# Kernel optimization log

Measured on AMD Instinct MI355X. Metric: run time of the kernel, lower is better.

The kernel has to match this reference:

```python
import jax, jax.numpy as jnp
import numpy as np

B, R, K, S = 512, 264, 32, 9
SUB_ENDS = np.array([28, 58, 92, 121, 150, 180, 210, 240, 264], dtype=np.int32)


def setup_inputs() -> dict:
    key = jax.random.key(0)
    embeddings = jax.random.normal(key, (B, R, K), dtype=jnp.float32)
    return {"embeddings": embeddings, "subnetwork_ends": jnp.asarray(SUB_ENDS)}


def reference(embeddings, subnetwork_ends):
    # subnetwork_ends are static structural constants (cumulative block ends).
    ends = np.asarray(jax.device_get(subnetwork_ends))
    starts = np.concatenate([np.zeros(1, dtype=ends.dtype), ends[:-1]])
    sizes = ends - starts                      # [S]
    n_sub = ends.shape[0]
    seg = np.repeat(np.arange(n_sub), sizes)   # [R] segment id per ROI

    # adjacency: batched gram matrix, [B, R, R]
    adjacency = jnp.einsum('brk,bpk->brp', embeddings, embeddings)

    # intra-network adjacency: zero out cross-block entries
    intra_mask = jnp.asarray(seg[:, None] == seg[None, :])  # [R, R] bool
    intra = adjacency * intra_mask                          # [B, R, R]

    # inter-network matrix: block means via one fused segment reduce
    # (replaces the O(S^2) per-block slice+mean loop in the original)
    one_hot = jnp.asarray(np.eye(n_sub, dtype=np.float32)[seg])          # [R, S]
    counts = jnp.asarray((sizes[:, None] * sizes[None, :]).astype(np.float32))  # [S, S]
    inter = jnp.einsum('brp,rs,pt->bst', adjacency, one_hot, one_hot) / counts  # [B, S, S]

    return intra[..., None], inter[..., None], adjacency[..., None]
```

## Files before the change

### kernel.cpp

```cpp
#include <hip/hip_runtime.h>


constexpr int B_ = 512, R_ = 264, K_ = 32, S_ = 9;
constexpr int RP_ = 292;
constexpr long long NI_ = (long long)B_ * R_ * R_;
constexpr long long NS_ = (long long)B_ * S_ * S_;

typedef float vf4 __attribute__((ext_vector_type(4)));

__global__ __launch_bounds__(576, 8) void adj_intra(
    const float* __restrict__ emb, float* __restrict__ out) {
  __shared__ float Et[K_ * RP_];
  __shared__ unsigned char seg_lut[288];

  const int b = blockIdx.x;
  const int stripe = blockIdx.y;
  const int tid = threadIdx.x;
  const float* __restrict__ eb = emb + (size_t)b * R_ * K_;

  for (int idx = tid; idx < (R_ * K_) / 4; idx += 576) {
    const int r = idx >> 3;
    const int kq = (idx & 7) * 4;
    const vf4 v = *reinterpret_cast<const vf4*>(eb + r * K_ + kq);
    Et[(kq + 0) * RP_ + r] = v.x;
    Et[(kq + 1) * RP_ + r] = v.y;
    Et[(kq + 2) * RP_ + r] = v.z;
    Et[(kq + 3) * RP_ + r] = v.w;
  }
  for (int z = tid; z < K_ * 24; z += 576) {
    const int k = z / 24, r = 264 + z % 24;
    Et[k * RP_ + r] = 0.0f;
  }
  if (tid < 288) {
    const int x = tid;
    seg_lut[x] = (x >= 28) + (x >= 58) + (x >= 92) + (x >= 121) +
                 (x >= 150) + (x >= 180) + (x >= 210) + (x >= 240);
  }
  __syncthreads();

  const int wave = tid >> 6, lane = tid & 63;
  const int lx = lane & 7, ly = lane >> 3;
  const int i0 = stripe * 32 + ly * 4;
  const int j0 = wave * 32 + lx * 4;

  vf4 acc0 = {0, 0, 0, 0}, acc1 = {0, 0, 0, 0};
  vf4 acc2 = {0, 0, 0, 0}, acc3 = {0, 0, 0, 0};
#pragma unroll 4
  for (int k = 0; k < K_; ++k) {
    const vf4 av = *reinterpret_cast<const vf4*>(Et + k * RP_ + i0);
    const vf4 bv = *reinterpret_cast<const vf4*>(Et + k * RP_ + j0);
    acc0 += av.x * bv;
    acc1 += av.y * bv;
    acc2 += av.z * bv;
    acc3 += av.w * bv;
  }

  if (j0 < R_) {
    float* __restrict__ intra_out = out;
    float* __restrict__ adj_out = out + NI_ + NS_;
    const int sj0 = seg_lut[j0], sj1 = seg_lut[j0 + 1];
    const int sj2 = seg_lut[j0 + 2], sj3 = seg_lut[j0 + 3];
    const size_t base = (size_t)b * R_ * R_ + (size_t)j0;
    const vf4 accs[4] = {acc0, acc1, acc2, acc3};
#pragma unroll
    for (int ii = 0; ii < 4; ++ii) {
      const int i = i0 + ii;
      if (i < R_) {
        const vf4 v = accs[ii];
        const int si = seg_lut[i];
        vf4 m;
        m.x = (si == sj0) ? v.x : 0.0f;
        m.y = (si == sj1) ? v.y : 0.0f;
        m.z = (si == sj2) ? v.z : 0.0f;
        m.w = (si == sj3) ? v.w : 0.0f;
        const size_t idx = base + (size_t)i * R_;
        __builtin_nontemporal_store(v, reinterpret_cast<vf4*>(adj_out + idx));
        __builtin_nontemporal_store(m, reinterpret_cast<vf4*>(intra_out + idx));
      }
    }
  }
}

__global__ __launch_bounds__(256) void inter_k(
    const float* __restrict__ emb, float* __restrict__ out) {
  constexpr int ENDS[S_] = {28, 58, 92, 121, 150, 180, 210, 240, 264};
  constexpr int STARTS[S_] = {0, 28, 58, 92, 121, 150, 180, 210, 240};
  constexpr float SZ[S_] = {28.f, 30.f, 34.f, 29.f, 29.f, 30.f, 30.f, 30.f, 24.f};

  __shared__ float ps[S_ * 8 * 32];
  __shared__ float ss[32 * 12];

  const int b = blockIdx.x, tid = threadIdx.x;
  const int k = tid & 31, q = tid >> 5;
  const float* __restrict__ eb = emb + (size_t)b * R_ * K_;

#pragma unroll
  for (int s = 0; s < S_; ++s) {
    const int lo = STARTS[s], len = ENDS[s] - STARTS[s];
    const int c0 = lo + (len * q) / 8, c1 = lo + (len * (q + 1)) / 8;
    float a = 0.0f;
    for (int r = c0; r < c1; ++r) a += eb[r * K_ + k];
    ps[(s * 8 + q) * 32 + k] = a;
  }
  __syncthreads();
  for (int c = tid; c < S_ * 32; c += 256) {
    const int s = c >> 5, kk = c & 31;
    float a = 0.0f;
#pragma unroll
    for (int qq = 0; qq < 8; ++qq) a += ps[(s * 8 + qq) * 32 + kk];
    ss[kk * 12 + s] = a;
  }
  __syncthreads();
  if (tid < S_ * S_) {
    const int s = tid / S_, t = tid % S_;
    float d = 0.0f;
    for (int kk = 0; kk < 32; ++kk) d += ss[kk * 12 + s] * ss[kk * 12 + t];
    d /= (SZ[s] * SZ[t]);
    __builtin_nontemporal_store(d, out + NI_ + (size_t)b * (S_ * S_) + tid);
  }
}

extern "C" void kernel_launch(void* const* d_in, const int* in_sizes, int n_in,
                              void* d_out, int out_size, void* d_ws,
                              size_t ws_size, hipStream_t stream) {
  const float* emb = (const float*)d_in[0];
  float* out = (float*)d_out;
  hipLaunchKernelGGL(adj_intra, dim3(B_, 9), dim3(576), 0, stream, emb, out);
  hipLaunchKernelGGL(inter_k, dim3(B_), dim3(256), 0, stream, emb, out);
}
```

Measured before the change: 389.3 us.

## Compute gram matrix with bf16 MFMA tiles instead of FP32 FMA

Converts the per-batch embeddings to bf16 in shared memory and computes 16x16 output tiles with the mfma_f32_16x16x32_bf16 instruction. The grid changes to 5 stripes of 512 threads. Stores become plain scalar stores instead of vectorized nontemporal ones. The kernel is dominated by writing about 285 MB of output, so the compute savings may be small, and bf16 inputs lose precision that may break tolerance. The narrower scalar stores may also reduce write efficiency.

Result: faster. 356.2 us (-8.5%).

```diff
diff --git a/kernel.cpp b/kernel.cpp
--- a/kernel.cpp
+++ b/kernel.cpp
@@ -2,36 +2,41 @@
 
 
 constexpr int B_ = 512, R_ = 264, K_ = 32, S_ = 9;
-constexpr int RP_ = 292;
+constexpr int LDR_ = 40;
 constexpr long long NI_ = (long long)B_ * R_ * R_;
 constexpr long long NS_ = (long long)B_ * S_ * S_;
 
+typedef float f32x4 __attribute__((ext_vector_type(4)));
 typedef float vf4 __attribute__((ext_vector_type(4)));
+typedef short bf16x8 __attribute__((ext_vector_type(8)));
 
-__global__ __launch_bounds__(576, 8) void adj_intra(
+static __device__ inline unsigned short f2bf(float f) {
+  unsigned int u = __builtin_bit_cast(unsigned int, f);
+  u += 0x7fffu + ((u >> 16) & 1u);
+  return (unsigned short)(u >> 16);
+}
+
+__global__ __launch_bounds__(512, 8) void adj_intra_mfma(
     const float* __restrict__ emb, float* __restrict__ out) {
-  __shared__ float Et[K_ * RP_];
-  __shared__ unsigned char seg_lut[288];
+  __shared__ unsigned short Ebf[272 * LDR_];
+  __shared__ unsigned char seg_lut[272];
 
   const int b = blockIdx.x;
   const int stripe = blockIdx.y;
   const int tid = threadIdx.x;
   const float* __restrict__ eb = emb + (size_t)b * R_ * K_;
 
-  for (int idx = tid; idx < (R_ * K_) / 4; idx += 576) {
+  for (int idx = tid; idx < (R_ * K_) / 4; idx += 512) {
     const int r = idx >> 3;
-    const int kq = (idx & 7) * 4;
-    const vf4 v = *reinterpret_cast<const vf4*>(eb + r * K_ + kq);
-    Et[(kq + 0) * RP_ + r] = v.x;
-    Et[(kq + 1) * RP_ + r] = v.y;
-    Et[(kq + 2) * RP_ + r] = v.z;
-    Et[(kq + 3) * RP_ + r] = v.w;
+    const int k4 = (idx & 7) * 4;
+    const f32x4 v = *reinterpret_cast<const f32x4*>(eb + r * K_ + k4);
+    const unsigned int lo = (unsigned int)f2bf(v.x) | ((unsigned int)f2bf(v.y) << 16);
+    const unsigned int hi = (unsigned int)f2bf(v.z) | ((unsigned int)f2bf(v.w) << 16);
+    uint2 pk; pk.x = lo; pk.y = hi;
+    *reinterpret_cast<uint2*>(&Ebf[r * LDR_ + k4]) = pk;
   }
-  for (int z = tid; z < K_ * 24; z += 576) {
-    const int k = z / 24, r = 264 + z % 24;
-    Et[k * RP_ + r] = 0.0f;
-  }
-  if (tid < 288) {
+  if (tid < 8 * LDR_) Ebf[264 * LDR_ + tid] = 0;
+  if (tid < 272) {
     const int x = tid;
     seg_lut[x] = (x >= 28) + (x >= 58) + (x >= 92) + (x >= 121) +
                  (x >= 150) + (x >= 180) + (x >= 210) + (x >= 240);
@@ -39,43 +44,38 @@
   __syncthreads();
 
   const int wave = tid >> 6, lane = tid & 63;
-  const int lx = lane & 7, ly = lane >> 3;
-  const int i0 = stripe * 32 + ly * 4;
-  const int j0 = wave * 32 + lx * 4;
+  const int half = lane >> 4;
+  const int l15 = lane & 15;
 
-  vf4 acc0 = {0, 0, 0, 0}, acc1 = {0, 0, 0, 0};
-  vf4 acc2 = {0, 0, 0, 0}, acc3 = {0, 0, 0, 0};
-#pragma unroll 4
-  for (int k = 0; k < K_; ++k) {
-    const vf4 av = *reinterpret_cast<const vf4*>(Et + k * RP_ + i0);
-    const vf4 bv = *reinterpret_cast<const vf4*>(Et + k * RP_ + j0);
-    acc0 += av.x * bv;
-    acc1 += av.y * bv;
-    acc2 += av.z * bv;
-    acc3 += av.w * bv;
-  }
+  const int ntiles = (stripe < 4) ? 4 * 17 : 17;
+  float* __restrict__ intra_out = out;
+  float* __restrict__ adj_out = out + NI_ + NS_;
+  const size_t bbase = (size_t)b * ((long long)R_ * R_);
 
-  if (j0 < R_) {
-    float* __restrict__ intra_out = out;
-    float* __restrict__ adj_out = out + NI_ + NS_;
-    const int sj0 = seg_lut[j0], sj1 = seg_lut[j0 + 1];
-    const int sj2 = seg_lut[j0 + 2], sj3 = seg_lut[j0 + 3];
-    const size_t base = (size_t)b * R_ * R_ + (size_t)j0;
-    const vf4 accs[4] = {acc0, acc1, acc2, acc3};
+  for (int t = wave; t < ntiles; t += 8) {
+    const int tr = stripe * 4 + t / 17;
+    const int tc = t % 17;
+    const bf16x8 af = *reinterpret_cast<const bf16x8*>(
+        &Ebf[(tr * 16 + l15) * LDR_ + half * 8]);
+    const bf16x8 bfr = *reinterpret_cast<const bf16x8*>(
+        &Ebf[(tc * 16 + l15) * LDR_ + half * 8]);
+    f32x4 acc = {0.f, 0.f, 0.f, 0.f};
+    acc = __builtin_amdgcn_mfma_f32_16x16x32_bf16(af, bfr, acc, 0, 0, 0);
+
+    const int j = tc * 16 + l15;
+    if (j < R_) {
+      const int sj = seg_lut[j];
+      const int ibase = tr * 16 + half * 4;
+      const size_t obase = bbase + (size_t)ibase * R_ + j;
 #pragma unroll
-    for (int ii = 0; ii < 4; ++ii) {
-      const int i = i0 + ii;
-      if (i < R_) {
-        const vf4 v = accs[ii];
-        const int si = seg_lut[i];
-        vf4 m;
-        m.x = (si == sj0) ? v.x : 0.0f;
-        m.y = (si == sj1) ? v.y : 0.0f;
-        m.z = (si == sj2) ? v.z : 0.0f;
-        m.w = (si == sj3) ? v.w : 0.0f;
-        const size_t idx = base + (size_t)i * R_;
-        __builtin_nontemporal_store(v, reinterpret_cast<vf4*>(adj_out + idx));
-        __builtin_nontemporal_store(m, reinterpret_cast<vf4*>(intra_out + idx));
+      for (int q = 0; q < 4; ++q) {
+        const int i = ibase + q;
+        if (i < R_) {
+          const float v = acc[q];
+          const int si = seg_lut[i];
+          adj_out[obase + (size_t)q * R_] = v;
+          intra_out[obase + (size_t)q * R_] = (si == sj) ? v : 0.0f;
+        }
       }
     }
   }
@@ -116,7 +116,7 @@
     float d = 0.0f;
     for (int kk = 0; kk < 32; ++kk) d += ss[kk * 12 + s] * ss[kk * 12 + t];
     d /= (SZ[s] * SZ[t]);
-    __builtin_nontemporal_store(d, out + NI_ + (size_t)b * (S_ * S_) + tid);
+    out[NI_ + (size_t)b * (S_ * S_) + tid] = d;
   }
 }
 
@@ -125,6 +125,6 @@
                               size_t ws_size, hipStream_t stream) {
   const float* emb = (const float*)d_in[0];
   float* out = (float*)d_out;
-  hipLaunchKernelGGL(adj_intra, dim3(B_, 9), dim3(576), 0, stream, emb, out);
+  hipLaunchKernelGGL(adj_intra_mfma, dim3(B_, 5), dim3(512), 0, stream, emb, out);
   hipLaunchKernelGGL(inter_k, dim3(B_), dim3(256), 0, stream, emb, out);
 }
```
